# Performance work log

Hardware: AMD Instinct MI355X
Metric: run time of the kernel (lower is better)

## Reference

```python
import jax, jax.numpy as jnp
import numpy as np

N, K = 8192, 133
N_LAYERS = 6
HID = 64
# mmpose RealNVP coupling masks: [0,1],[1,0] repeated 3 times
MASK = jnp.array([[0.0, 1.0], [1.0, 0.0]] * 3, dtype=jnp.float32)  # [6,2]


def _mlp(x, w1, b1, w2, b2, w3, b3):
    # x: [P,2] -> [P,2]; LeakyReLU slope 0.01 (torch default)
    h = jax.nn.leaky_relu(x @ w1.T + b1, 0.01)
    h = jax.nn.leaky_relu(h @ w2.T + b2, 0.01)
    return h @ w3.T + b3


def _flow_log_prob(x, s_w1, s_b1, s_w2, s_b2, s_w3, s_b3,
                   t_w1, t_b1, t_w2, t_b2, t_w3, t_b3):
    # RealNVP backward pass: x -> z, accumulating log-det Jacobian
    z = x
    log_det = jnp.zeros(x.shape[0], x.dtype)
    for i in reversed(range(N_LAYERS)):
        m = MASK[i]
        z_ = m * z
        s = jnp.tanh(_mlp(z_, s_w1[i], s_b1[i], s_w2[i], s_b2[i], s_w3[i], s_b3[i])) * (1.0 - m)
        t = _mlp(z_, t_w1[i], t_b1[i], t_w2[i], t_b2[i], t_w3[i], t_b3[i]) * (1.0 - m)
        z = (1.0 - m) * (z - t) * jnp.exp(-s) + z_
        log_det = log_det - s.sum(axis=1)
    # standard 2D normal prior log-prob
    prior_lp = -0.5 * jnp.sum(z * z, axis=1) - jnp.log(2.0 * jnp.pi)
    return prior_lp + log_det


def setup_inputs() -> dict:
    key = jax.random.key(0)
    ks = jax.random.split(key, 16)
    inp = {
        'pred': jax.random.normal(ks[0], (N, K, 4), dtype=jnp.float32),
        'target': jax.random.normal(ks[1], (N, K, 2), dtype=jnp.float32),
        'target_weight': jax.random.uniform(ks[2], (N, K), dtype=jnp.float32),
    }
    dims = [(HID, 2), (HID,), (HID, HID), (HID,), (2, HID), (2,)]
    names = ['w1', 'b1', 'w2', 'b2', 'w3', 'b3']
    kidx = 3
    for pfx in ('s', 't'):
        for nm, d in zip(names, dims):
            inp[f'{pfx}_{nm}'] = 0.1 * jax.random.normal(ks[kidx], (N_LAYERS,) + d, dtype=jnp.float32)
            kidx += 1
    return inp


def reference(pred, target, target_weight,
              s_w1, s_b1, s_w2, s_b2, s_w3, s_b3,
              t_w1, t_b1, t_w2, t_b2, t_w3, t_b3):
    miu = pred[:, :, :2]
    sigma = jnp.sqrt(jnp.abs(pred[:, :, 2:4]))  # sigmoid=False
    error = (miu - target) / (sigma + 1e-9)  # [N,K,2]
    log_phi = _flow_log_prob(error.reshape(-1, 2),
                             s_w1, s_b1, s_w2, s_b2, s_w3, s_b3,
                             t_w1, t_b1, t_w2, t_b2, t_w3, t_b3)
    log_phi = log_phi.reshape(pred.shape[0], pred.shape[1], 1)
    log_sigma = jnp.log(sigma)
    nf_loss = log_sigma - log_phi  # [N,K,2]
    # residual=True, q_distribution='laplace'
    loss_q = jnp.log(sigma * 2.0) + jnp.abs(error)
    loss = nf_loss + loss_q
    loss = loss * target_weight[:, :, None]  # use_target_weight=True
    loss = loss / pred.shape[0]  # size_average=True: divide by len(loss)=N
    return loss.sum()
```

## Files before the change

### kernel.cpp

```cpp
#include <hip/hip_runtime.h>

typedef __attribute__((ext_vector_type(8))) short bfrag_t;
typedef __attribute__((ext_vector_type(4))) float f4_t;
typedef __attribute__((ext_vector_type(4))) unsigned u4_t;

#define LOG_2PI   1.8378770664093453f
#define TWO_LOG2  1.3862943611198906f
#define T_TILES   8
#define BLOCK     256
#define PTS_BLK   512

__device__ __forceinline__ unsigned pkbf(float lo, float hi) {
  unsigned r;
  asm("v_cvt_pk_bf16_f32 %0, %1, %2" : "=v"(r) : "v"(lo), "v"(hi));
  return r;
}
__device__ __forceinline__ float leaky(float h) { return fmaxf(h, 0.01f * h); }

__device__ __forceinline__ void stage_layer(u4_t* afr, const float* sW2, const float* tW2,
                                            int layer, int tid) {
  #pragma unroll
  for (int it = 0; it < 4; ++it) {
    int idx = tid + it * BLOCK;
    int l = idx & 63, f = (idx >> 6) & 7, m = (idx >> 9) & 1;
    int n = f & 3, q = f >> 2;
    int row = 16 * n + (l & 15), kb = 32 * q + 8 * (l >> 4);
    const float* src = (m ? tW2 : sW2) + layer * 4096 + row * 64 + kb;
    float4 a = *(const float4*)src;
    float4 b = *(const float4*)(src + 4);
    afr[(m * 8 + f) * 64 + l] =
        (u4_t){pkbf(a.x, a.y), pkbf(a.z, a.w), pkbf(b.x, b.y), pkbf(b.z, b.w)};
  }
}

__global__ __launch_bounds__(BLOCK)
void ihll_kernel(
    const float* __restrict__ pred, const float* __restrict__ targ, const float* __restrict__ twp,
    const float* __restrict__ sW1, const float* __restrict__ sB1, const float* __restrict__ sW2,
    const float* __restrict__ sB2, const float* __restrict__ sW3, const float* __restrict__ sB3,
    const float* __restrict__ tW1, const float* __restrict__ tB1, const float* __restrict__ tW2,
    const float* __restrict__ tB2, const float* __restrict__ tW3, const float* __restrict__ tB3,
    float* __restrict__ out, int M) {
  __shared__ u4_t   afr[2 * 8 * 64];
  __shared__ float4 zld[PTS_BLK];
  __shared__ float  pre0v[PTS_BLK];
  __shared__ float  c1s[6][2][64];
  __shared__ float  b1s[6][2][64];
  __shared__ unsigned wbs[6][2][64];
  __shared__ float  wsum[4];

  const int tid  = threadIdx.x;
  const int lane = tid & 63, wave = tid >> 6;
  const int pr   = lane & 15, g = lane >> 4;
  const int pbase = blockIdx.x * PTS_BLK;

  for (int idx = tid; idx < 768; idx += BLOCK) {
    int i = idx >> 7, r = idx & 127, m = r >> 6, j = r & 63;
    int jo = i & 1, jm = jo ^ 1;
    const float* w1 = m ? tW1 : sW1;  const float* b1 = m ? tB1 : sB1;
    const float* w3 = m ? tW3 : sW3;  const float* b2 = m ? tB2 : sB2;
    c1s[i][m][j] = w1[i * 128 + j * 2 + jm];
    b1s[i][m][j] = b1[i * 64 + j];
    wbs[i][m][j] = pkbf(b2[i * 64 + j], w3[i * 128 + jo * 64 + j]);
  }
  #pragma unroll
  for (int it = 0; it < 2; ++it) {
    int idx = tid + it * BLOCK;
    int P = pbase + idx;
    float4 zs = make_float4(0.f, 0.f, 0.f, 0.f);
    if (P < M) {
      float4 p4 = ((const float4*)pred)[P];
      float2 t2 = ((const float2*)targ)[P];
      float s0 = sqrtf(fabsf(p4.z)), s1 = sqrtf(fabsf(p4.w));
      zs.x = (p4.x - t2.x) / (s0 + 1e-9f);
      zs.y = (p4.y - t2.y) / (s1 + 1e-9f);
    }
    zld[idx] = zs;
  }
  stage_layer(afr, sW2, tW2, 5, tid);
  __syncthreads();

  const int wbase = wave * (T_TILES * 16);

  #pragma unroll 1
  for (int li = 0; li < 6; ++li) {
    const int i = 5 - li;
    const int jo = i & 1;
    const bool upd0 = (jo == 0);
    const float b3s = sB3[i * 2 + jo];
    const float b3t = tB3[i * 2 + jo];

    #pragma unroll 1
    for (int m = 0; m < 2; ++m) {
      u4_t af[8];
      #pragma unroll
      for (int f = 0; f < 8; ++f)
        af[f] = afr[(m * 8 + f) * 64 + lane];

      f4_t c1q[4], b1q[4];
      #pragma unroll
      for (int q = 0; q < 2; ++q) {
        c1q[2 * q]     = *(const f4_t*)&c1s[i][m][q * 32 + 8 * g];
        c1q[2 * q + 1] = *(const f4_t*)&c1s[i][m][q * 32 + 8 * g + 4];
        b1q[2 * q]     = *(const f4_t*)&b1s[i][m][q * 32 + 8 * g];
        b1q[2 * q + 1] = *(const f4_t*)&b1s[i][m][q * 32 + 8 * g + 4];
      }
      f4_t b2u[4], w3u[4];
      #pragma unroll
      for (int n = 0; n < 4; ++n) {
        u4_t wv = *(const u4_t*)&wbs[i][m][n * 16 + 4 * g];
        #pragma unroll
        for (int r = 0; r < 4; ++r) {
          b2u[n][r] = __uint_as_float(wv[r] << 16);
          w3u[n][r] = __uint_as_float(wv[r] & 0xffff0000u);
        }
      }

      #pragma unroll 1
      for (int t = 0; t < T_TILES; ++t) {
        const int widx = wbase + t * 16 + pr;
        float4 zv = zld[widx];
        const float zin = upd0 ? zv.y : zv.x;

        f4_t acc[4];
        #pragma unroll
        for (int q = 0; q < 2; ++q) {
          const f4_t ca = c1q[2 * q], cb = c1q[2 * q + 1];
          const f4_t ba = b1q[2 * q], bb = b1q[2 * q + 1];
          float h0 = leaky(fmaf(ca[0], zin, ba[0]));
          float h1 = leaky(fmaf(ca[1], zin, ba[1]));
          float h2 = leaky(fmaf(ca[2], zin, ba[2]));
          float h3 = leaky(fmaf(ca[3], zin, ba[3]));
          float h4 = leaky(fmaf(cb[0], zin, bb[0]));
          float h5 = leaky(fmaf(cb[1], zin, bb[1]));
          float h6 = leaky(fmaf(cb[2], zin, bb[2]));
          float h7 = leaky(fmaf(cb[3], zin, bb[3]));
          bfrag_t B = __builtin_bit_cast(bfrag_t,
              make_uint4(pkbf(h0, h1), pkbf(h2, h3), pkbf(h4, h5), pkbf(h6, h7)));
          #pragma unroll
          for (int n = 0; n < 4; ++n) {
            f4_t c = (q == 0) ? b2u[n] : acc[n];
            acc[n] = __builtin_amdgcn_mfma_f32_16x16x32_bf16(
                __builtin_bit_cast(bfrag_t, af[q * 4 + n]), B, c, 0, 0, 0);
          }
        }
        float pa = 0.f;
        #pragma unroll
        for (int n = 0; n < 4; ++n)
          #pragma unroll
          for (int r = 0; r < 4; ++r)
            pa = fmaf(leaky(acc[n][r]), w3u[n][r], pa);
        pa += __shfl_xor(pa, 16);
        pa += __shfl_xor(pa, 32);

        if (m == 0) {
          if (g == 0) pre0v[widx] = pa;
        } else {
          float p0  = pre0v[widx];
          float sv  = 1.f - 2.f / (__expf(2.f * (p0 + b3s)) + 1.f);
          float tv  = pa + b3t;
          float zo  = upd0 ? zv.x : zv.y;
          float zn  = (zo - tv) * __expf(-sv);
          if (upd0) zv.x = zn; else zv.y = zn;
          zv.z -= sv;
          if (g == 0) zld[widx] = zv;
        }
      }
    }
    __syncthreads();
    if (li < 5) {
      stage_layer(afr, sW2, tW2, i - 1, tid);
      __syncthreads();
    }
  }

  float csum = 0.f;
  #pragma unroll
  for (int it = 0; it < 2; ++it) {
    int idx = tid + it * BLOCK;
    int P = pbase + idx;
    if (P < M) {
      float4 p4 = ((const float4*)pred)[P];
      float2 t2 = ((const float2*)targ)[P];
      float w   = twp[P];
      float s0 = sqrtf(fabsf(p4.z)), s1 = sqrtf(fabsf(p4.w));
      float e0 = (p4.x - t2.x) / (s0 + 1e-9f);
      float e1 = (p4.y - t2.y) / (s1 + 1e-9f);
      float bs = 2.f * (logf(s0) + logf(s1)) + TWO_LOG2 + fabsf(e0) + fabsf(e1);
      float4 zv = zld[idx];
      float prior = -0.5f * (zv.x * zv.x + zv.y * zv.y) - LOG_2PI;
      float lphi  = prior + zv.z;
      csum += (bs - 2.f * lphi) * w;
    }
  }
  #pragma unroll
  for (int off = 1; off <= 32; off <<= 1)
    csum += __shfl_xor(csum, off);
  if (lane == 0) wsum[wave] = csum;
  __syncthreads();
  if (tid == 0) {
    float tot = wsum[0] + wsum[1] + wsum[2] + wsum[3];
    atomicAdd(out, tot * (1.0f / 8192.0f));
  }
}

extern "C" void kernel_launch(void* const* d_in, const int* in_sizes, int n_in,
                              void* d_out, int out_size, void* d_ws, size_t ws_size,
                              hipStream_t stream) {
  const float* pred = (const float*)d_in[0];
  const float* targ = (const float*)d_in[1];
  const float* twp  = (const float*)d_in[2];
  const float* sW1 = (const float*)d_in[3];  const float* sB1 = (const float*)d_in[4];
  const float* sW2 = (const float*)d_in[5];  const float* sB2 = (const float*)d_in[6];
  const float* sW3 = (const float*)d_in[7];  const float* sB3 = (const float*)d_in[8];
  const float* tW1 = (const float*)d_in[9];  const float* tB1 = (const float*)d_in[10];
  const float* tW2 = (const float*)d_in[11]; const float* tB2 = (const float*)d_in[12];
  const float* tW3 = (const float*)d_in[13]; const float* tB3 = (const float*)d_in[14];

  const int M = in_sizes[2];
  const int blocks = (M + PTS_BLK - 1) / PTS_BLK;

  hipMemsetAsync(d_out, 0, sizeof(float), stream);
  hipLaunchKernelGGL(ihll_kernel, dim3(blocks), dim3(BLOCK), 0, stream,
                     pred, targ, twp, sW1, sB1, sW2, sB2, sW3, sB3,
                     tW1, tB1, tW2, tB2, tW3, tB3, (float*)d_out, M);
}
```

Before: 271.9 us.

## Switch flow MLP to packed fp16 math with f16 MFMA and dot2 epilogue

```diff
diff --git a/kernel.cpp b/kernel.cpp
--- a/kernel.cpp
+++ b/kernel.cpp
@@ -1,7 +1,8 @@
 #include <hip/hip_runtime.h>
 
-typedef __attribute__((ext_vector_type(8))) short bfrag_t;
-typedef __attribute__((ext_vector_type(4))) float f4_t;
+typedef _Float16 hfrag_t __attribute__((ext_vector_type(8)));
+typedef _Float16 h2_t    __attribute__((ext_vector_type(2)));
+typedef __attribute__((ext_vector_type(4))) float    f4_t;
 typedef __attribute__((ext_vector_type(4))) unsigned u4_t;
 
 #define LOG_2PI   1.8378770664093453f
@@ -9,13 +10,25 @@
 #define T_TILES   8
 #define BLOCK     256
 #define PTS_BLK   512
-
-__device__ __forceinline__ unsigned pkbf(float lo, float hi) {
-  unsigned r;
-  asm("v_cvt_pk_bf16_f32 %0, %1, %2" : "=v"(r) : "v"(lo), "v"(hi));
+#define ZCLAMP    30000.0f
+
+__device__ __forceinline__ unsigned pkh(float a, float b) {
+  return __builtin_bit_cast(unsigned, __builtin_amdgcn_cvt_pkrtz(a, b));
+}
+__device__ __forceinline__ unsigned pk_fma_h(unsigned a, unsigned b, unsigned c) {
+  unsigned d;
+  asm("v_pk_fma_f16 %0, %1, %2, %3" : "=v"(d) : "v"(a), "v"(b), "v"(c));
+  return d;
+}
+__device__ __forceinline__ unsigned pk_leaky_h(unsigned h, unsigned k01) {
+  unsigned t, r;
+  asm("v_pk_mul_f16 %0, %1, %2" : "=v"(t) : "v"(h), "v"(k01));
+  asm("v_pk_max_f16 %0, %1, %2" : "=v"(r) : "v"(h), "v"(t));
   return r;
 }
-__device__ __forceinline__ float leaky(float h) { return fmaxf(h, 0.01f * h); }
+__device__ __forceinline__ float dot2h(unsigned a, unsigned b, float c) {
+  return __builtin_amdgcn_fdot2(__builtin_bit_cast(h2_t, a), __builtin_bit_cast(h2_t, b), c, false);
+}
 
 __device__ __forceinline__ void stage_layer(u4_t* afr, const float* sW2, const float* tW2,
                                             int layer, int tid) {
@@ -29,7 +42,7 @@
     float4 a = *(const float4*)src;
     float4 b = *(const float4*)(src + 4);
     afr[(m * 8 + f) * 64 + l] =
-        (u4_t){pkbf(a.x, a.y), pkbf(a.z, a.w), pkbf(b.x, b.y), pkbf(b.z, b.w)};
+        (u4_t){pkh(a.x, a.y), pkh(a.z, a.w), pkh(b.x, b.y), pkh(b.z, b.w)};
   }
 }
 
@@ -41,27 +54,40 @@
     const float* __restrict__ tW1, const float* __restrict__ tB1, const float* __restrict__ tW2,
     const float* __restrict__ tB2, const float* __restrict__ tW3, const float* __restrict__ tB3,
     float* __restrict__ out, int M) {
-  __shared__ u4_t   afr[2 * 8 * 64];
-  __shared__ float4 zld[PTS_BLK];
-  __shared__ float  pre0v[PTS_BLK];
-  __shared__ float  c1s[6][2][64];
-  __shared__ float  b1s[6][2][64];
-  __shared__ unsigned wbs[6][2][64];
-  __shared__ float  wsum[4];
+  __shared__ u4_t     afr[2 * 8 * 64];
+  __shared__ float4   zld[PTS_BLK];
+  __shared__ float    pre0v[PTS_BLK];
+  __shared__ unsigned c1h[6][2][32];
+  __shared__ unsigned b1h[6][2][32];
+  __shared__ unsigned w3h[6][2][4][8];
+  __shared__ float    b2s[6][2][64];
+  __shared__ float    wsum[4];
 
   const int tid  = threadIdx.x;
   const int lane = tid & 63, wave = tid >> 6;
   const int pr   = lane & 15, g = lane >> 4;
   const int pbase = blockIdx.x * PTS_BLK;
-
+  const unsigned k01h = pkh(0.01f, 0.01f);
+
+  for (int idx = tid; idx < 384; idx += BLOCK) {
+    int i = idx >> 6, r = idx & 63, m = r >> 5, jp = r & 31;
+    int jo = i & 1, jm = jo ^ 1;
+    const float* w1 = m ? tW1 : sW1;  const float* b1 = m ? tB1 : sB1;
+    c1h[i][m][jp] = pkh(w1[i * 128 + 4 * jp + jm], w1[i * 128 + 4 * jp + 2 + jm]);
+    b1h[i][m][jp] = pkh(b1[i * 64 + 2 * jp], b1[i * 64 + 2 * jp + 1]);
+  }
+  for (int idx = tid; idx < 384; idx += BLOCK) {
+    int i = idx >> 6, r = idx & 63, m = r >> 5, c = r & 31;
+    int gg = c >> 3, c2 = c & 7, n = c2 >> 1, jj = c2 & 1;
+    int jo = i & 1;
+    const float* w3 = m ? tW3 : sW3;
+    int row = 16 * n + 4 * gg + 2 * jj;
+    w3h[i][m][gg][c2] = pkh(w3[i * 128 + jo * 64 + row], w3[i * 128 + jo * 64 + row + 1]);
+  }
   for (int idx = tid; idx < 768; idx += BLOCK) {
     int i = idx >> 7, r = idx & 127, m = r >> 6, j = r & 63;
-    int jo = i & 1, jm = jo ^ 1;
-    const float* w1 = m ? tW1 : sW1;  const float* b1 = m ? tB1 : sB1;
-    const float* w3 = m ? tW3 : sW3;  const float* b2 = m ? tB2 : sB2;
-    c1s[i][m][j] = w1[i * 128 + j * 2 + jm];
-    b1s[i][m][j] = b1[i * 64 + j];
-    wbs[i][m][j] = pkbf(b2[i * 64 + j], w3[i * 128 + jo * 64 + j]);
+    const float* b2 = m ? tB2 : sB2;
+    b2s[i][m][j] = b2[i * 64 + j];
   }
   #pragma unroll
   for (int it = 0; it < 2; ++it) {
@@ -81,6 +107,7 @@
   __syncthreads();
 
   const int wbase = wave * (T_TILES * 16);
+  const float* zldf = (const float*)zld;
 
   #pragma unroll 1
   for (int li = 0; li < 6; ++li) {
@@ -90,66 +117,58 @@
     const float b3s = sB3[i * 2 + jo];
     const float b3t = tB3[i * 2 + jo];
 
-    #pragma unroll 1
+    #pragma unroll
     for (int m = 0; m < 2; ++m) {
       u4_t af[8];
       #pragma unroll
       for (int f = 0; f < 8; ++f)
         af[f] = afr[(m * 8 + f) * 64 + lane];
-
-      f4_t c1q[4], b1q[4];
+      unsigned c1q[8], b1q[8];
+      *(u4_t*)&c1q[0] = *(const u4_t*)&c1h[i][m][4 * g];
+      *(u4_t*)&c1q[4] = *(const u4_t*)&c1h[i][m][16 + 4 * g];
+      *(u4_t*)&b1q[0] = *(const u4_t*)&b1h[i][m][4 * g];
+      *(u4_t*)&b1q[4] = *(const u4_t*)&b1h[i][m][16 + 4 * g];
+      unsigned w3q[8];
+      *(u4_t*)&w3q[0] = *(const u4_t*)&w3h[i][m][g][0];
+      *(u4_t*)&w3q[4] = *(const u4_t*)&w3h[i][m][g][4];
+      f4_t b2q[4];
       #pragma unroll
-      for (int q = 0; q < 2; ++q) {
-        c1q[2 * q]     = *(const f4_t*)&c1s[i][m][q * 32 + 8 * g];
-        c1q[2 * q + 1] = *(const f4_t*)&c1s[i][m][q * 32 + 8 * g + 4];
-        b1q[2 * q]     = *(const f4_t*)&b1s[i][m][q * 32 + 8 * g];
-        b1q[2 * q + 1] = *(const f4_t*)&b1s[i][m][q * 32 + 8 * g + 4];
-      }
-      f4_t b2u[4], w3u[4];
-      #pragma unroll
-      for (int n = 0; n < 4; ++n) {
-        u4_t wv = *(const u4_t*)&wbs[i][m][n * 16 + 4 * g];
-        #pragma unroll
-        for (int r = 0; r < 4; ++r) {
-          b2u[n][r] = __uint_as_float(wv[r] << 16);
-          w3u[n][r] = __uint_as_float(wv[r] & 0xffff0000u);
-        }
-      }
+      for (int n = 0; n < 4; ++n)
+        b2q[n] = *(const f4_t*)&b2s[i][m][n * 16 + 4 * g];
 
       #pragma unroll 1
       for (int t = 0; t < T_TILES; ++t) {
         const int widx = wbase + t * 16 + pr;
-        float4 zv = zld[widx];
-        const float zin = upd0 ? zv.y : zv.x;
+        float4 zv;
+        float zin;
+        if (m == 1) { zv = zld[widx]; zin = upd0 ? zv.y : zv.x; }
+        else        { zin = zldf[4 * widx + (upd0 ? 1 : 0)]; }
+        float zc = fmaxf(fminf(zin, ZCLAMP), -ZCLAMP);
+        const unsigned zz = pkh(zc, zc);
 
         f4_t acc[4];
         #pragma unroll
         for (int q = 0; q < 2; ++q) {
-          const f4_t ca = c1q[2 * q], cb = c1q[2 * q + 1];
-          const f4_t ba = b1q[2 * q], bb = b1q[2 * q + 1];
-          float h0 = leaky(fmaf(ca[0], zin, ba[0]));
-          float h1 = leaky(fmaf(ca[1], zin, ba[1]));
-          float h2 = leaky(fmaf(ca[2], zin, ba[2]));
-          float h3 = leaky(fmaf(ca[3], zin, ba[3]));
-          float h4 = leaky(fmaf(cb[0], zin, bb[0]));
-          float h5 = leaky(fmaf(cb[1], zin, bb[1]));
-          float h6 = leaky(fmaf(cb[2], zin, bb[2]));
-          float h7 = leaky(fmaf(cb[3], zin, bb[3]));
-          bfrag_t B = __builtin_bit_cast(bfrag_t,
-              make_uint4(pkbf(h0, h1), pkbf(h2, h3), pkbf(h4, h5), pkbf(h6, h7)));
+          unsigned hh[4];
+          #pragma unroll
+          for (int e = 0; e < 4; ++e)
+            hh[e] = pk_leaky_h(pk_fma_h(c1q[q * 4 + e], zz, b1q[q * 4 + e]), k01h);
+          hfrag_t B = __builtin_bit_cast(hfrag_t, (u4_t){hh[0], hh[1], hh[2], hh[3]});
           #pragma unroll
           for (int n = 0; n < 4; ++n) {
-            f4_t c = (q == 0) ? b2u[n] : acc[n];
-            acc[n] = __builtin_amdgcn_mfma_f32_16x16x32_bf16(
-                __builtin_bit_cast(bfrag_t, af[q * 4 + n]), B, c, 0, 0, 0);
+            f4_t c = (q == 0) ? b2q[n] : acc[n];
+            acc[n] = __builtin_amdgcn_mfma_f32_16x16x32_f16(
+                __builtin_bit_cast(hfrag_t, af[q * 4 + n]), B, c, 0, 0, 0);
           }
         }
         float pa = 0.f;
         #pragma unroll
-        for (int n = 0; n < 4; ++n)
-          #pragma unroll
-          for (int r = 0; r < 4; ++r)
-            pa = fmaf(leaky(acc[n][r]), w3u[n][r], pa);
+        for (int n = 0; n < 4; ++n) {
+          unsigned x01 = pk_leaky_h(pkh(acc[n][0], acc[n][1]), k01h);
+          unsigned x23 = pk_leaky_h(pkh(acc[n][2], acc[n][3]), k01h);
+          pa = dot2h(x01, w3q[2 * n], pa);
+          pa = dot2h(x23, w3q[2 * n + 1], pa);
+        }
         pa += __shfl_xor(pa, 16);
         pa += __shfl_xor(pa, 32);
 
```

After: 232.0 us. 1.17x faster.
